# Optimization experiments

Measured on AMD Instinct MI355X. Metric: run time of the kernel, lower is better.

Reference implementation:

```python
import jax, jax.numpy as jnp
import numpy as np
import math

D_MODEL = 1024
NUM_HEADS = 16
D_K = D_MODEL // NUM_HEADS
B, S = 2, 2048


def setup_inputs() -> dict:
    key = jax.random.key(0)
    ks = jax.random.split(key, 13)
    scale = 1.0 / math.sqrt(D_MODEL)
    inp = {
        "q": jax.random.normal(ks[0], (B, S, D_MODEL), jnp.float32),
        "k": jax.random.normal(ks[1], (B, S, D_MODEL), jnp.float32),
        "v": jax.random.normal(ks[2], (B, S, D_MODEL), jnp.float32),
        "mask": jax.random.randint(ks[3], (B, 1, S, S), 0, 2, jnp.int32),
        # torch nn.Linear params: y = x @ W.T + b
        "wQ_w": jax.random.normal(ks[4], (D_MODEL, D_MODEL), jnp.float32) * scale,
        "wQ_b": jax.random.normal(ks[5], (D_MODEL,), jnp.float32) * scale,
        "wK_w": jax.random.normal(ks[6], (D_MODEL, D_MODEL), jnp.float32) * scale,
        "wK_b": jax.random.normal(ks[7], (D_MODEL,), jnp.float32) * scale,
        "wV_w": jax.random.normal(ks[8], (D_MODEL, D_MODEL), jnp.float32) * scale,
        "wV_b": jax.random.normal(ks[9], (D_MODEL,), jnp.float32) * scale,
        "wO_w": jax.random.normal(ks[10], (D_MODEL, D_MODEL), jnp.float32) * scale,
        "wO_b": jax.random.normal(ks[11], (D_MODEL,), jnp.float32) * scale,
    }
    return inp


def _split_heads(x):
    # [B, S, D] -> [B, H, S, dK]
    b, s, _ = x.shape
    return x.reshape(b, s, NUM_HEADS, D_K).transpose(0, 2, 1, 3)


def reference(q, k, v, mask, wQ_w, wQ_b, wK_w, wK_b, wV_w, wV_b, wO_w, wO_b):
    qh = _split_heads(q @ wQ_w.T + wQ_b)
    kh = _split_heads(k @ wK_w.T + wK_b)
    vh = _split_heads(v @ wV_w.T + wV_b)
    # scores: [B, H, S, S] -- materialized as in the original module
    scores = jnp.einsum("bhsd,bhtd->bhst", qh, kh) / math.sqrt(D_K)
    scores = jnp.where(mask == 0, jnp.float32(-1e9), scores)
    attn = jax.nn.softmax(scores, axis=-1)
    out = jnp.einsum("bhst,bhtd->bhsd", attn, vh)  # [B, H, S, dK]
    out = out.transpose(0, 2, 1, 3).reshape(q.shape[0], -1, D_MODEL)
    return out @ wO_w.T + wO_b
```

## Files before the change

kernel.cpp:

```cpp
#include <hip/hip_runtime.h>
#include <hip/hip_bf16.h>
#include <stdint.h>
#include <math.h>

#define NHEADS 16
#define DK 64
#define BATCH 2
#define SEQ 2048
#define DMODEL 1024
#define MROWS (BATCH*SEQ)

typedef __bf16 bf16x8 __attribute__((ext_vector_type(8)));
typedef float  f32x4  __attribute__((ext_vector_type(4)));
typedef float  f32x16 __attribute__((ext_vector_type(16)));

typedef const __attribute__((address_space(1))) void* gas_ptr;
typedef       __attribute__((address_space(3))) void* las_ptr;

__device__ __forceinline__ void async16(const void* g, void* l) {
  __builtin_amdgcn_global_load_lds((gas_ptr)g, (las_ptr)l, 16, 0, 0);
}

__device__ __forceinline__ unsigned short f2bf_raw(float f) {
  __hip_bfloat16 h = __float2bfloat16(f);
  return *reinterpret_cast<unsigned short*>(&h);
}

__device__ __forceinline__ float fast_exp2(float x) {
#if __has_builtin(__builtin_amdgcn_exp2f)
  return __builtin_amdgcn_exp2f(x);
#else
  float r;
  asm("v_exp_f32 %0, %1\ns_nop 1" : "=v"(r) : "v"(x));
  return r;
#endif
}

__device__ __forceinline__ uint32_t pk_bf16(float lo, float hi2) {
  uint32_t r;
  asm("v_cvt_pk_bf16_f32 %0, %1, %2" : "=v"(r) : "v"(lo), "v"(hi2));
  return r;
}

__device__ __forceinline__ void half_swap(uint32_t& a, uint32_t& b) {
  auto r = __builtin_amdgcn_permlane32_swap(a, b, false, false);
  a = (uint32_t)r[0];
  b = (uint32_t)r[1];
}

__device__ __forceinline__ float mask_sel(uint32_t msel, float s, float c) {
  uint32_t su = __float_as_uint(s), cu = __float_as_uint(c);
  return __uint_as_float((msel & su) | (~msel & cu));
}

__device__ __forceinline__ f32x16 zero16() {
  f32x16 z;
#pragma unroll
  for (int i = 0; i < 16; ++i) z[i] = 0.f;
  return z;
}

__global__ void prep_kernel(const float* __restrict__ q,
                            const float* __restrict__ k,
                            const float* __restrict__ v,
                            const float* __restrict__ w0,
                            const float* __restrict__ w1,
                            const float* __restrict__ w2,
                            const float* __restrict__ w3,
                            ushort4* __restrict__ out,
                            const int* __restrict__ mask,
                            uint32_t* __restrict__ bits) {
  if (blockIdx.x < 16384) {
    int i = blockIdx.x * 256 + threadIdx.x;
    const float* src;
    int local;
    if (i < 3145728) {
      int seg = i >> 20;
      src = (seg == 0) ? q : (seg == 1) ? k : v;
      local = i & 1048575;
    } else {
      int j = i - 3145728;
      int seg = j >> 18;
      src = (seg == 0) ? w0 : (seg == 1) ? w1 : (seg == 2) ? w2 : w3;
      local = j & 262143;
    }
    float4 f = reinterpret_cast<const float4*>(src)[local];
    ushort4 u;
    u.x = f2bf_raw(f.x); u.y = f2bf_raw(f.y);
    u.z = f2bf_raw(f.z); u.w = f2bf_raw(f.w);
    out[i] = u;
  } else {
    int i = (blockIdx.x - 16384) * 256 + threadIdx.x;
    unsigned long long bal = __ballot(mask[i] != 0);
    int lane = threadIdx.x & 63;
    if (lane == 0)  bits[i >> 5] = (uint32_t)bal;
    if (lane == 32) bits[i >> 5] = (uint32_t)(bal >> 32);
  }
}


__device__ __forceinline__ void gemm_core_128(
    const __hip_bfloat16* __restrict__ A, const __hip_bfloat16* __restrict__ Bw,
    int K, int m0, int n0,
    __hip_bfloat16* sA, __hip_bfloat16* sB, f32x4 acc[4][4]) {
  const int lane = threadIdx.x & 63;
  const int wid  = threadIdx.x >> 6;
  const int wr = wid >> 1, wc = wid & 1;
  const int l15 = lane & 15, lg = lane >> 4;
  const int sw = l15 & 7;
  const int crow8 = lane >> 3;
  const int cslot = lane & 7;

#pragma unroll
  for (int mi = 0; mi < 4; ++mi)
#pragma unroll
    for (int ni = 0; ni < 4; ++ni) acc[mi][ni] = f32x4{0.f, 0.f, 0.f, 0.f};

  for (int k0 = 0; k0 < K; k0 += 64) {
#pragma unroll
    for (int c0 = 0; c0 < 4; ++c0) {
      int c = wid + c0 * 4;
      int row = c * 8 + crow8;
      int scol = (cslot ^ (row & 7)) * 8;
      async16(A  + (size_t)(m0 + row) * K + k0 + scol,
              (char*)sA + c * 1024 + lane * 16);
      async16(Bw + (size_t)(n0 + row) * K + k0 + scol,
              (char*)sB + c * 1024 + lane * 16);
    }
    __syncthreads();
#pragma unroll
    for (int kc = 0; kc < 2; ++kc) {
      bf16x8 af[4], bfr[4];
#pragma unroll
      for (int mi = 0; mi < 4; ++mi)
        af[mi] = *reinterpret_cast<const bf16x8*>(
            &sA[(wr * 64 + mi * 16 + l15) * 64 + (((kc * 4 + lg) ^ sw) * 8)]);
#pragma unroll
      for (int ni = 0; ni < 4; ++ni)
        bfr[ni] = *reinterpret_cast<const bf16x8*>(
            &sB[(wc * 64 + ni * 16 + l15) * 64 + (((kc * 4 + lg) ^ sw) * 8)]);
      __builtin_amdgcn_s_setprio(1);
#pragma unroll
      for (int mi = 0; mi < 4; ++mi)
#pragma unroll
        for (int ni = 0; ni < 4; ++ni)
          acc[mi][ni] = __builtin_amdgcn_mfma_f32_16x16x32_bf16(
              af[mi], bfr[ni], acc[mi][ni], 0, 0, 0);
      __builtin_amdgcn_s_setprio(0);
    }
    __syncthreads();
  }
}

__global__ __launch_bounds__(256, 3) void qkv_gemm_kernel(
    const __hip_bfloat16* __restrict__ Xq, const __hip_bfloat16* __restrict__ Xk,
    const __hip_bfloat16* __restrict__ Xv,
    const __hip_bfloat16* __restrict__ Wq, const __hip_bfloat16* __restrict__ Wk,
    const __hip_bfloat16* __restrict__ Wv,
    const float* __restrict__ bq, const float* __restrict__ bk,
    const float* __restrict__ bv,
    __hip_bfloat16* __restrict__ Qh, __hip_bfloat16* __restrict__ Kh,
    __hip_bfloat16* __restrict__ VhT) {
  __shared__ __hip_bfloat16 sA[128 * 64];
  __shared__ __hip_bfloat16 sB[128 * 64];
  const int z = blockIdx.z;
  const __hip_bfloat16* A  = (z == 0) ? Xq : (z == 1) ? Xk : Xv;
  const __hip_bfloat16* Bw = (z == 0) ? Wq : (z == 1) ? Wk : Wv;
  const float* bias        = (z == 0) ? bq : (z == 1) ? bk : bv;
  __hip_bfloat16* Co       = (z == 0) ? Qh : (z == 1) ? Kh : VhT;
  const int m0 = blockIdx.x * 128, n0 = blockIdx.y * 128;
  f32x4 acc[4][4];
  gemm_core_128(A, Bw, DMODEL, m0, n0, sA, sB, acc);

  const int lane = threadIdx.x & 63, wid = threadIdx.x >> 6;
  const int wr = wid >> 1, wc = wid & 1;
  const int l15 = lane & 15, lg = lane >> 4;
  const float osc = (z == 0) ? 0.18033688f : 1.0f;
  if (z != 2) {
#pragma unroll
    for (int mi = 0; mi < 4; ++mi)
#pragma unroll
      for (int ni = 0; ni < 4; ++ni) {
        int j = n0 + wc * 64 + ni * 16 + l15;
        float bj = bias[j];
        int hh = j >> 6, d = j & 63;
#pragma unroll
        for (int r = 0; r < 4; ++r) {
          int i = m0 + wr * 64 + mi * 16 + lg * 4 + r;
          int bb = i >> 11, s = i & 2047;
          float v = (acc[mi][ni][r] + bj) * osc;
          Co[((size_t)(bb * NHEADS + hh) * SEQ + s) * DK + d] = __float2bfloat16(v);
        }
      }
  } else {
#pragma unroll
    for (int mi = 0; mi < 4; ++mi)
#pragma unroll
      for (int ni = 0; ni < 4; ++ni) {
        int j = n0 + wc * 64 + ni * 16 + l15;
        float bj = bias[j];
        int hh = j >> 6, d = j & 63;
        int i0 = m0 + wr * 64 + mi * 16 + lg * 4;
        int bb = i0 >> 11, sbase = i0 & 2047;
        ushort4 st;
        st.x = f2bf_raw(acc[mi][ni][0] + bj);
        st.y = f2bf_raw(acc[mi][ni][1] + bj);
        st.z = f2bf_raw(acc[mi][ni][2] + bj);
        st.w = f2bf_raw(acc[mi][ni][3] + bj);
        *reinterpret_cast<ushort4*>(
            &Co[((size_t)(bb * NHEADS + hh) * DK + d) * SEQ + sbase]) = st;
      }
  }
}

__global__ __launch_bounds__(256, 3) void out_gemm_kernel(
    const __hip_bfloat16* __restrict__ A, const __hip_bfloat16* __restrict__ Ww,
    const float* __restrict__ bias, float* __restrict__ C) {
  __shared__ __hip_bfloat16 sA[128 * 64];
  __shared__ __hip_bfloat16 sB[128 * 64];
  const int m0 = blockIdx.x * 128, n0 = blockIdx.y * 128;
  f32x4 acc[4][4];
  gemm_core_128(A, Ww, DMODEL, m0, n0, sA, sB, acc);
  const int lane = threadIdx.x & 63, wid = threadIdx.x >> 6;
  const int wr = wid >> 1, wc = wid & 1;
#pragma unroll
  for (int mi = 0; mi < 4; ++mi)
#pragma unroll
    for (int ni = 0; ni < 4; ++ni) {
      int j = n0 + wc * 64 + ni * 16 + (lane & 15);
      float bj = bias[j];
#pragma unroll
      for (int r = 0; r < 4; ++r) {
        int i = m0 + wr * 64 + mi * 16 + (lane >> 4) * 4 + r;
        C[(size_t)i * DMODEL + j] = acc[mi][ni][r] + bj;
      }
    }
}


__global__ __launch_bounds__(512, 4) void attn_kernel(
    const __hip_bfloat16* __restrict__ Qh, const __hip_bfloat16* __restrict__ Kh,
    const __hip_bfloat16* __restrict__ VhT, const uint32_t* __restrict__ mbits,
    __hip_bfloat16* __restrict__ AO) {
  __shared__ char pool[65536 + 512 + 512];
  __hip_bfloat16* Kpool = (__hip_bfloat16*)pool;
  __hip_bfloat16* Vpool = (__hip_bfloat16*)(pool + 32768);
  float* sRed = (float*)(pool + 65536);
  float* lC   = (float*)(pool + 65536 + 512);
  float* accC = (float*)pool;

  const int tid = threadIdx.x, lane = tid & 63, wid = tid >> 6;
  const int grp = wid >> 2, wq = wid & 3;
  const int ltid = tid & 255;
  const int l31 = lane & 31, hi = lane >> 5;
  const int sw = l31 & 7;
  const int bh = blockIdx.y, b = bh >> 4, h = bh & 15;
  const int q0g = blockIdx.x * 128 + wq * 32;
  const int kvbase = grp * (SEQ / 2);

  const __hip_bfloat16* Qp = Qh  + (size_t)bh * SEQ * DK;
  const __hip_bfloat16* Kp = Kh  + (size_t)bh * SEQ * DK;
  const __hip_bfloat16* Vp = VhT + (size_t)bh * DK * SEQ;
  const uint32_t* mb = mbits + (size_t)b * SEQ * (SEQ / 32)
                             + (size_t)(q0g + l31) * (SEQ / 32) + (kvbase >> 5);
  float* sRedW = &sRed[wq * 32];

  bf16x8 qf[4];
#pragma unroll
  for (int dc = 0; dc < 4; ++dc)
    qf[dc] = *reinterpret_cast<const bf16x8*>(
        &Qp[(size_t)(q0g + l31) * DK + dc * 16 + hi * 8]);

  f32x16 acc0 = zero16(), acc1 = zero16();
  float l_run = 0.f;

#define STAGE(kv0_, s_)                                                        \
  {                                                                            \
    _Pragma("unroll")                                                          \
    for (int u = 0; u < 2; ++u) {                                              \
      int c = ltid + u * 256;                                                  \
      int row = c >> 3, ss = (c & 7) ^ (row & 7);                              \
      async16(Kp + (size_t)(kvbase + (kv0_) + row) * DK + ss * 8,              \
              (char*)(Kpool + (grp * 2 + (s_)) * 4096) + c * 16);              \
      async16(Vp + (size_t)row * SEQ + kvbase + (kv0_) + ss * 8,               \
              (char*)(Vpool + (grp * 2 + (s_)) * 4096) + c * 16);              \
    }                                                                          \
  }

  STAGE(0, 0);
  uint2 mw = *reinterpret_cast<const uint2*>(mb);
  asm volatile("s_waitcnt vmcnt(0)" ::: "memory");
  __syncthreads();

  const int NT = SEQ / 2 / 64;
  for (int t = 0; t < NT; ++t) {
    const int cur = t & 1;
    if (t + 1 < NT) STAGE((t + 1) * 64, cur ^ 1);

    uint2 mw_next;
    if (t + 1 < NT) mw_next = *reinterpret_cast<const uint2*>(mb + (t + 1) * 2);
    uint32_t w0 = mw.x >> (4 * hi), w1 = mw.y >> (4 * hi);

    const __hip_bfloat16* ks = Kpool + (grp * 2 + cur) * 4096;
    const __hip_bfloat16* vs = Vpool + (grp * 2 + cur) * 4096;

    f32x16 s0 = zero16(), s1 = zero16();
    __builtin_amdgcn_s_setprio(1);
#pragma unroll
    for (int dc = 0; dc < 4; ++dc) {
      bf16x8 k0 = *reinterpret_cast<const bf16x8*>(
          &ks[(size_t)(l31) * 64 + (((dc * 2 + hi) ^ sw) * 8)]);
      bf16x8 k1 = *reinterpret_cast<const bf16x8*>(
          &ks[(size_t)(32 + l31) * 64 + (((dc * 2 + hi) ^ sw) * 8)]);
      s0 = __builtin_amdgcn_mfma_f32_32x32x16_bf16(k0, qf[dc], s0, 0, 0, 0);
      s1 = __builtin_amdgcn_mfma_f32_32x32x16_bf16(k1, qf[dc], s1, 0, 0, 0);
    }
    __builtin_amdgcn_s_setprio(0);

    union { uint32_t u[4]; bf16x8 v; } pc;
    {
      float p[16];
#pragma unroll
      for (int r = 0; r < 16; ++r) {
        const int sh = (r & 3) + 8 * (r >> 2);
        uint32_t msel = (uint32_t)__builtin_amdgcn_sbfe((int)w0, sh, 1);
        p[r] = fast_exp2(mask_sel(msel, s0[r], -1e9f));
        l_run += p[r];
      }
      uint32_t a0 = pk_bf16(p[0], p[1]),  a1 = pk_bf16(p[2], p[3]);
      uint32_t b0 = pk_bf16(p[4], p[5]),  b1 = pk_bf16(p[6], p[7]);
      uint32_t c0 = pk_bf16(p[8], p[9]),  c1 = pk_bf16(p[10], p[11]);
      uint32_t d0 = pk_bf16(p[12], p[13]), d1 = pk_bf16(p[14], p[15]);
      half_swap(a0, b0); half_swap(a1, b1);
      half_swap(c0, d0); half_swap(c1, d1);
      __builtin_amdgcn_s_setprio(1);
      pc.u[0] = a0; pc.u[1] = a1; pc.u[2] = b0; pc.u[3] = b1;
      {
        bf16x8 v0 = *reinterpret_cast<const bf16x8*>(
            &vs[(size_t)(l31) * 64 + (((0 + hi) ^ sw) * 8)]);
        bf16x8 v1 = *reinterpret_cast<const bf16x8*>(
            &vs[(size_t)(32 + l31) * 64 + (((0 + hi) ^ sw) * 8)]);
        acc0 = __builtin_amdgcn_mfma_f32_32x32x16_bf16(pc.v, v0, acc0, 0, 0, 0);
        acc1 = __builtin_amdgcn_mfma_f32_32x32x16_bf16(pc.v, v1, acc1, 0, 0, 0);
      }
      pc.u[0] = c0; pc.u[1] = c1; pc.u[2] = d0; pc.u[3] = d1;
      {
        bf16x8 v0 = *reinterpret_cast<const bf16x8*>(
            &vs[(size_t)(l31) * 64 + (((2 + hi) ^ sw) * 8)]);
        bf16x8 v1 = *reinterpret_cast<const bf16x8*>(
            &vs[(size_t)(32 + l31) * 64 + (((2 + hi) ^ sw) * 8)]);
        acc0 = __builtin_amdgcn_mfma_f32_32x32x16_bf16(pc.v, v0, acc0, 0, 0, 0);
        acc1 = __builtin_amdgcn_mfma_f32_32x32x16_bf16(pc.v, v1, acc1, 0, 0, 0);
      }
      __builtin_amdgcn_s_setprio(0);
    }
    {
      float p[16];
#pragma unroll
      for (int r = 0; r < 16; ++r) {
        const int sh = (r & 3) + 8 * (r >> 2);
        uint32_t msel = (uint32_t)__builtin_amdgcn_sbfe((int)w1, sh, 1);
        p[r] = fast_exp2(mask_sel(msel, s1[r], -1e9f));
        l_run += p[r];
      }
      uint32_t a0 = pk_bf16(p[0], p[1]),  a1 = pk_bf16(p[2], p[3]);
      uint32_t b0 = pk_bf16(p[4], p[5]),  b1 = pk_bf16(p[6], p[7]);
      uint32_t c0 = pk_bf16(p[8], p[9]),  c1 = pk_bf16(p[10], p[11]);
      uint32_t d0 = pk_bf16(p[12], p[13]), d1 = pk_bf16(p[14], p[15]);
      half_swap(a0, b0); half_swap(a1, b1);
      half_swap(c0, d0); half_swap(c1, d1);
      __builtin_amdgcn_s_setprio(1);
      pc.u[0] = a0; pc.u[1] = a1; pc.u[2] = b0; pc.u[3] = b1;
      {
        bf16x8 v0 = *reinterpret_cast<const bf16x8*>(
            &vs[(size_t)(l31) * 64 + (((4 + hi) ^ sw) * 8)]);
        bf16x8 v1 = *reinterpret_cast<const bf16x8*>(
            &vs[(size_t)(32 + l31) * 64 + (((4 + hi) ^ sw) * 8)]);
        acc0 = __builtin_amdgcn_mfma_f32_32x32x16_bf16(pc.v, v0, acc0, 0, 0, 0);
        acc1 = __builtin_amdgcn_mfma_f32_32x32x16_bf16(pc.v, v1, acc1, 0, 0, 0);
      }
      pc.u[0] = c0; pc.u[1] = c1; pc.u[2] = d0; pc.u[3] = d1;
      {
        bf16x8 v0 = *reinterpret_cast<const bf16x8*>(
            &vs[(size_t)(l31) * 64 + (((6 + hi) ^ sw) * 8)]);
        bf16x8 v1 = *reinterpret_cast<const bf16x8*>(
            &vs[(size_t)(32 + l31) * 64 + (((6 + hi) ^ sw) * 8)]);
        acc0 = __builtin_amdgcn_mfma_f32_32x32x16_bf16(pc.v, v0, acc0, 0, 0, 0);
        acc1 = __builtin_amdgcn_mfma_f32_32x32x16_bf16(pc.v, v1, acc1, 0, 0, 0);
      }
      __builtin_amdgcn_s_setprio(0);
    }

    mw = mw_next;
    asm volatile("s_waitcnt vmcnt(0)" ::: "memory");
    __syncthreads();
  }

  l_run += __shfl_xor(l_run, 32);

  if (grp == 1) {
    float* myacc = &accC[(wq * 64 + lane) * 32];
#pragma unroll
    for (int r = 0; r < 16; ++r) { myacc[r] = acc0[r]; myacc[16 + r] = acc1[r]; }
    if (hi == 0) lC[wq * 32 + l31] = l_run;
  }
  __syncthreads();

  if (grp == 0) {
    const float* oacc = &accC[(wq * 64 + lane) * 32];
#pragma unroll
    for (int r = 0; r < 16; ++r) { acc0[r] += oacc[r]; acc1[r] += oacc[16 + r]; }
    float l_tot = l_run + lC[wq * 32 + l31];
    if (hi == 0) sRedW[l31] = l_tot;
    asm volatile("s_waitcnt lgkmcnt(0)" ::: "memory");
#pragma unroll
    for (int r = 0; r < 16; ++r) {
      int cr = (r & 3) + 8 * (r >> 2) + 4 * hi;
      float linv = 1.0f / sRedW[cr];
      int qrow = q0g + cr;
      size_t base = ((size_t)b * SEQ + qrow) * DMODEL + h * 64 + l31;
      AO[base]      = __float2bfloat16(acc0[r] * linv);
      AO[base + 32] = __float2bfloat16(acc1[r] * linv);
    }
  }
}


extern "C" void kernel_launch(void* const* d_in, const int* in_sizes, int n_in,
                              void* d_out, int out_size, void* d_ws, size_t ws_size,
                              hipStream_t stream) {
  const float* q    = (const float*)d_in[0];
  const float* k    = (const float*)d_in[1];
  const float* v    = (const float*)d_in[2];
  const int*   mask = (const int*)d_in[3];
  const float* wQ_w = (const float*)d_in[4];
  const float* wQ_b = (const float*)d_in[5];
  const float* wK_w = (const float*)d_in[6];
  const float* wK_b = (const float*)d_in[7];
  const float* wV_w = (const float*)d_in[8];
  const float* wV_b = (const float*)d_in[9];
  const float* wO_w = (const float*)d_in[10];
  const float* wO_b = (const float*)d_in[11];

  char* ws = (char*)d_ws;
  const size_t SZ_X = (size_t)MROWS * DMODEL * 2;
  const size_t SZ_W = (size_t)DMODEL * DMODEL * 2;
  __hip_bfloat16* Xq  = (__hip_bfloat16*)(ws);
  __hip_bfloat16* Xk  = (__hip_bfloat16*)(ws + SZ_X);
  __hip_bfloat16* Xv  = (__hip_bfloat16*)(ws + 2 * SZ_X);
  __hip_bfloat16* Wq  = (__hip_bfloat16*)(ws + 3 * SZ_X);
  __hip_bfloat16* Wk  = (__hip_bfloat16*)(ws + 3 * SZ_X + SZ_W);
  __hip_bfloat16* Wv  = (__hip_bfloat16*)(ws + 3 * SZ_X + 2 * SZ_W);
  __hip_bfloat16* Wo  = (__hip_bfloat16*)(ws + 3 * SZ_X + 3 * SZ_W);
  __hip_bfloat16* Qh  = (__hip_bfloat16*)(ws + 3 * SZ_X + 4 * SZ_W);
  __hip_bfloat16* Kh  = (__hip_bfloat16*)(ws + 4 * SZ_X + 4 * SZ_W);
  __hip_bfloat16* VhT = (__hip_bfloat16*)(ws + 5 * SZ_X + 4 * SZ_W);
  __hip_bfloat16* AO  = (__hip_bfloat16*)(ws + 6 * SZ_X + 4 * SZ_W);
  uint32_t*       MB  = (uint32_t*)      (ws + 7 * SZ_X + 4 * SZ_W);

  prep_kernel<<<49152, 256, 0, stream>>>(q, k, v, wQ_w, wK_w, wV_w, wO_w,
                                         (ushort4*)ws, mask, MB);

  qkv_gemm_kernel<<<dim3(MROWS / 128, DMODEL / 128, 3), 256, 0, stream>>>(
      Xq, Xk, Xv, Wq, Wk, Wv, wQ_b, wK_b, wV_b, Qh, Kh, VhT);

  attn_kernel<<<dim3(SEQ / 128, BATCH * NHEADS), 512, 0, stream>>>(
      Qh, Kh, VhT, MB, AO);

  out_gemm_kernel<<<dim3(MROWS / 128, DMODEL / 128), 256, 0, stream>>>(
      AO, Wo, wO_b, (float*)d_out);
}
```

Before: 250.6 us.

## Stage QKV GEMM epilogue through LDS and vectorize mask bit-packing

The QKV projection epilogue now writes results into a padded LDS tile and then emits 16-byte vectorized global stores for both the head-split Q/K layout and the transposed V layout, replacing scattered 2-byte and 8-byte stores. Separately, the mask packing path reads int4 vectors per lane and combines nibbles with shuffles, so each block handles four times more mask elements and the prep grid is halved. The cost is larger shared memory in the QKV kernel plus an extra barrier, which may affect occupancy.

```diff
diff --git a/kernel.cpp b/kernel.cpp
--- a/kernel.cpp
+++ b/kernel.cpp
@@ -90,11 +90,17 @@
     u.z = f2bf_raw(f.z); u.w = f2bf_raw(f.w);
     out[i] = u;
   } else {
-    int i = (blockIdx.x - 16384) * 256 + threadIdx.x;
-    unsigned long long bal = __ballot(mask[i] != 0);
-    int lane = threadIdx.x & 63;
-    if (lane == 0)  bits[i >> 5] = (uint32_t)bal;
-    if (lane == 32) bits[i >> 5] = (uint32_t)(bal >> 32);
+    int bi = blockIdx.x - 16384;
+    int lane = threadIdx.x & 63, wid = threadIdx.x >> 6;
+    size_t base = (size_t)bi * 1024 + (size_t)wid * 256;
+    int4 q4 = reinterpret_cast<const int4*>(mask + base)[lane];
+    uint32_t nib = (q4.x != 0 ? 1u : 0u) | (q4.y != 0 ? 2u : 0u) |
+                   (q4.z != 0 ? 4u : 0u) | (q4.w != 0 ? 8u : 0u);
+    nib <<= (lane & 7) * 4;
+    nib |= (uint32_t)__shfl_xor((int)nib, 1);
+    nib |= (uint32_t)__shfl_xor((int)nib, 2);
+    nib |= (uint32_t)__shfl_xor((int)nib, 4);
+    if ((lane & 7) == 0) bits[(base >> 5) + (lane >> 3)] = nib;
   }
 }
 
@@ -161,8 +167,9 @@
     const float* __restrict__ bv,
     __hip_bfloat16* __restrict__ Qh, __hip_bfloat16* __restrict__ Kh,
     __hip_bfloat16* __restrict__ VhT) {
-  __shared__ __hip_bfloat16 sA[128 * 64];
-  __shared__ __hip_bfloat16 sB[128 * 64];
+  __shared__ __attribute__((aligned(16))) char smem[128 * 136 * 2];
+  __hip_bfloat16* sA = (__hip_bfloat16*)smem;
+  __hip_bfloat16* sB = (__hip_bfloat16*)(smem + 16384);
   const int z = blockIdx.z;
   const __hip_bfloat16* A  = (z == 0) ? Xq : (z == 1) ? Xk : Xv;
   const __hip_bfloat16* Bw = (z == 0) ? Wq : (z == 1) ? Wk : Wv;
@@ -172,52 +179,72 @@
   f32x4 acc[4][4];
   gemm_core_128(A, Bw, DMODEL, m0, n0, sA, sB, acc);
 
-  const int lane = threadIdx.x & 63, wid = threadIdx.x >> 6;
+  const int tid = threadIdx.x, lane = tid & 63, wid = tid >> 6;
   const int wr = wid >> 1, wc = wid & 1;
   const int l15 = lane & 15, lg = lane >> 4;
   const float osc = (z == 0) ? 0.18033688f : 1.0f;
+  const int PITCH = 136;
+  __hip_bfloat16* sT = (__hip_bfloat16*)smem;
+
   if (z != 2) {
 #pragma unroll
     for (int mi = 0; mi < 4; ++mi)
 #pragma unroll
       for (int ni = 0; ni < 4; ++ni) {
-        int j = n0 + wc * 64 + ni * 16 + l15;
-        float bj = bias[j];
-        int hh = j >> 6, d = j & 63;
+        int jl = wc * 64 + ni * 16 + l15;
+        float bj = bias[n0 + jl];
 #pragma unroll
         for (int r = 0; r < 4; ++r) {
-          int i = m0 + wr * 64 + mi * 16 + lg * 4 + r;
-          int bb = i >> 11, s = i & 2047;
-          float v = (acc[mi][ni][r] + bj) * osc;
-          Co[((size_t)(bb * NHEADS + hh) * SEQ + s) * DK + d] = __float2bfloat16(v);
+          int il = wr * 64 + mi * 16 + lg * 4 + r;
+          sT[il * PITCH + jl] = __float2bfloat16((acc[mi][ni][r] + bj) * osc);
         }
       }
+    __syncthreads();
+#pragma unroll
+    for (int u = 0; u < 8; ++u) {
+      int t2 = tid + u * 256;
+      int row = t2 >> 4, c8 = (t2 & 15) * 8;
+      bf16x8 val = *reinterpret_cast<const bf16x8*>(&sT[row * PITCH + c8]);
+      int ig = m0 + row, jg = n0 + c8;
+      int bb = ig >> 11, s = ig & 2047, hh = jg >> 6, d = jg & 63;
+      *reinterpret_cast<bf16x8*>(
+          &Co[((size_t)(bb * NHEADS + hh) * SEQ + s) * DK + d]) = val;
+    }
   } else {
 #pragma unroll
     for (int mi = 0; mi < 4; ++mi)
 #pragma unroll
       for (int ni = 0; ni < 4; ++ni) {
-        int j = n0 + wc * 64 + ni * 16 + l15;
-        float bj = bias[j];
-        int hh = j >> 6, d = j & 63;
-        int i0 = m0 + wr * 64 + mi * 16 + lg * 4;
-        int bb = i0 >> 11, sbase = i0 & 2047;
-        ushort4 st;
-        st.x = f2bf_raw(acc[mi][ni][0] + bj);
-        st.y = f2bf_raw(acc[mi][ni][1] + bj);
-        st.z = f2bf_raw(acc[mi][ni][2] + bj);
-        st.w = f2bf_raw(acc[mi][ni][3] + bj);
-        *reinterpret_cast<ushort4*>(
-            &Co[((size_t)(bb * NHEADS + hh) * DK + d) * SEQ + sbase]) = st;
-      }
+        int jl = wc * 64 + ni * 16 + l15;
+        float bj = bias[n0 + jl];
+        int il0 = wr * 64 + mi * 16 + lg * 4;
+        ushort4 st4;
+        st4.x = f2bf_raw(acc[mi][ni][0] + bj);
+        st4.y = f2bf_raw(acc[mi][ni][1] + bj);
+        st4.z = f2bf_raw(acc[mi][ni][2] + bj);
+        st4.w = f2bf_raw(acc[mi][ni][3] + bj);
+        *reinterpret_cast<ushort4*>(&sT[jl * PITCH + il0]) = st4;
+      }
+    __syncthreads();
+#pragma unroll
+    for (int u = 0; u < 8; ++u) {
+      int t2 = tid + u * 256;
+      int row = t2 >> 4, i8 = (t2 & 15) * 8;
+      bf16x8 val = *reinterpret_cast<const bf16x8*>(&sT[row * PITCH + i8]);
+      int jg = n0 + row, hh = jg >> 6, d = jg & 63;
+      int ig0 = m0 + i8, bb = ig0 >> 11, s0 = ig0 & 2047;
+      *reinterpret_cast<bf16x8*>(
+          &Co[((size_t)(bb * NHEADS + hh) * DK + d) * SEQ + s0]) = val;
+    }
   }
 }
 
 __global__ __launch_bounds__(256, 3) void out_gemm_kernel(
     const __hip_bfloat16* __restrict__ A, const __hip_bfloat16* __restrict__ Ww,
     const float* __restrict__ bias, float* __restrict__ C) {
-  __shared__ __hip_bfloat16 sA[128 * 64];
-  __shared__ __hip_bfloat16 sB[128 * 64];
+  __shared__ __attribute__((aligned(16))) char smem[32768];
+  __hip_bfloat16* sA = (__hip_bfloat16*)smem;
+  __hip_bfloat16* sB = (__hip_bfloat16*)(smem + 16384);
   const int m0 = blockIdx.x * 128, n0 = blockIdx.y * 128;
   f32x4 acc[4][4];
   gemm_core_128(A, Ww, DMODEL, m0, n0, sA, sB, acc);
@@ -458,7 +485,7 @@
   __hip_bfloat16* AO  = (__hip_bfloat16*)(ws + 6 * SZ_X + 4 * SZ_W);
   uint32_t*       MB  = (uint32_t*)      (ws + 7 * SZ_X + 4 * SZ_W);
 
-  prep_kernel<<<49152, 256, 0, stream>>>(q, k, v, wQ_w, wK_w, wV_w, wO_w,
+  prep_kernel<<<24576, 256, 0, stream>>>(q, k, v, wQ_w, wK_w, wV_w, wO_w,
                                          (ushort4*)ws, mask, MB);
 
   qkv_gemm_kernel<<<dim3(MROWS / 128, DMODEL / 128, 3), 256, 0, stream>>>(
```

New measurement: 237.8 us. 1.05x faster.
